# Optimization experiments

Measured on AMD Instinct MI355X. Metric: run time of the kernel, lower is better.

Reference implementation:

```python
import jax, jax.numpy as jnp
import numpy as np

N_NODES = 50000
N_EDGES = 800000
D_IN = 128
D_OUT = 128
NUM_RELS = 100


def setup_inputs() -> dict:
    key = jax.random.key(0)
    k1, k2, k3, k4, k5, k6, k7 = jax.random.split(key, 7)
    h = jax.random.normal(k1, (N_NODES, D_IN), dtype=jnp.float32)
    W = jax.random.normal(k2, (D_IN, D_OUT), dtype=jnp.float32) * 0.05
    attn = jax.random.normal(k3, (2 * D_OUT,), dtype=jnp.float32) * 0.05
    rel_emb = jax.random.normal(k4, (NUM_RELS, 1), dtype=jnp.float32)
    src = jax.random.randint(k5, (N_EDGES,), 0, N_NODES, dtype=jnp.int32)
    dst = jax.random.randint(k6, (N_EDGES,), 0, N_NODES, dtype=jnp.int32)
    etype = jax.random.randint(k7, (N_EDGES,), 0, NUM_RELS, dtype=jnp.int32)
    return {"h": h, "W": W, "attn": attn, "rel_emb": rel_emb,
            "src": src, "dst": dst, "etype": etype}


def reference(h, W, attn, rel_emb, src, dst, etype):
    # h: [N, d_in], W: [d_in, d_out], attn: [2*d_out], rel_emb: [R, 1]
    # src/dst/etype: [E]
    N = h.shape[0]
    d = W.shape[1]
    # padding_idx=0 in nn.Embedding -> row 0 is zero
    rel_table = rel_emb.at[0].set(0.0)
    z = h @ W  # [N, d_out]
    # attn_fc([z_src, z_dst]) = z_src @ a_l + z_dst @ a_r (split the concat-linear)
    s_src = z @ attn[:d]  # [N]
    s_dst = z @ attn[d:]  # [N]
    e = jax.nn.leaky_relu(s_src[src] + s_dst[dst])  # [E], slope 0.01 as in torch
    # segment softmax over incoming edges of each dst node
    m = jax.ops.segment_max(e, dst, num_segments=N)  # [N]
    ex = jnp.exp(e - m[dst])  # [E]
    denom = jax.ops.segment_sum(ex, dst, num_segments=N)  # [N]
    alpha = ex / denom[dst]  # [E]
    coef = rel_table[etype, 0] * alpha  # [E]  (rel_alpha * alpha)
    # weighted sum of source messages per destination node
    out = jax.ops.segment_sum(coef[:, None] * z[src], dst, num_segments=N)  # [N, d_out]
    return out
```

## Files before the change

kernel.cpp:

```cpp
#include <hip/hip_runtime.h>

#define D 128
#define GROWS 64
#define SPLIT 16
#define NPP (256 / SPLIT)
#define MAXPART 512

typedef __attribute__((ext_vector_type(8))) short short8;
typedef __attribute__((ext_vector_type(4))) float float4v;

__device__ __forceinline__ ushort f2bf(float x) {
    uint u = __float_as_uint(x);
    return (ushort)((u + 0x7FFFu + ((u >> 16) & 1u)) >> 16);
}
__device__ __forceinline__ float bf_lo(uint u) { return __uint_as_float(u << 16); }
__device__ __forceinline__ float bf_hi(uint u) { return __uint_as_float(u & 0xFFFF0000u); }

__global__ __launch_bounds__(256) void convW_kernel(
    const float* __restrict__ W, ushort* __restrict__ Wtg)
{
    int idx = blockIdx.x * 256 + threadIdx.x;
    int k = idx >> 7, n = idx & 127;
    Wtg[n * 128 + k] = f2bf(W[idx]);
}

__global__ __launch_bounds__(512) void gemm_mfma_kernel(
    const float* __restrict__ h, const ushort* __restrict__ Wtg,
    const float* __restrict__ attn, const int* __restrict__ dst,
    ushort* __restrict__ zb, float* __restrict__ s_src, float* __restrict__ s_dst,
    int* __restrict__ histm, int nhi, int N, int E, int nblocks)
{
    __shared__ ushort ht[GROWS * 136];
    __shared__ float psum_s[GROWS][2];
    __shared__ float psum_d[GROWS][2];
    __shared__ int histA[256];
    const int tid = threadIdx.x;
    const int base = blockIdx.x * GROWS;

#pragma unroll
    for (int it = 0; it < 4; ++it) {
        int idx = it * 512 + tid;
        int r = idx >> 5, c4 = (idx & 31) * 4;
        float4 v = make_float4(0.f, 0.f, 0.f, 0.f);
        if (base + r < N) v = *(const float4*)&h[(size_t)(base + r) * D + c4];
        ushort4 u = make_ushort4(f2bf(v.x), f2bf(v.y), f2bf(v.z), f2bf(v.w));
        *(ushort4*)&ht[r * 136 + c4] = u;
    }
    if (tid < 256) histA[tid] = 0;
    __syncthreads();

    const int lane = tid & 63;
    const int wave = tid >> 6;
    const int wr = wave >> 1;
    const int wc = wave & 1;
    const int col = lane & 15;
    const int quad = lane >> 4;
    const int wm = wr * 16;

    float4v acc[4];
#pragma unroll
    for (int nt = 0; nt < 4; ++nt) acc[nt] = (float4v)(0.f);

#pragma unroll
    for (int kc = 0; kc < 128; kc += 32) {
        short8 a = *(const short8*)&ht[(wm + col) * 136 + kc + quad * 8];
#pragma unroll
        for (int nt = 0; nt < 4; ++nt) {
            short8 b = *(const short8*)&Wtg[(wc * 64 + nt * 16 + col) * 128 + kc + quad * 8];
            acc[nt] = __builtin_amdgcn_mfma_f32_16x16x32_bf16(a, b, acc[nt], 0, 0, 0);
        }
    }
    __syncthreads();

    float ps[4] = {0.f, 0.f, 0.f, 0.f}, pd[4] = {0.f, 0.f, 0.f, 0.f};
#pragma unroll
    for (int nt = 0; nt < 4; ++nt) {
        float aL = attn[wc * 64 + nt * 16 + col];
        float aR = attn[D + wc * 64 + nt * 16 + col];
#pragma unroll
        for (int reg = 0; reg < 4; ++reg) {
            float v = acc[nt][reg];
            ps[reg] = fmaf(v, aL, ps[reg]);
            pd[reg] = fmaf(v, aR, pd[reg]);
            ht[(wm + quad * 4 + reg) * 136 + wc * 64 + nt * 16 + col] = f2bf(v);
        }
    }
#pragma unroll
    for (int reg = 0; reg < 4; ++reg) {
#pragma unroll
        for (int off = 1; off < 16; off <<= 1) {
            ps[reg] += __shfl_xor(ps[reg], off);
            pd[reg] += __shfl_xor(pd[reg], off);
        }
        if (col == 0) {
            int rl = wm + quad * 4 + reg;
            psum_s[rl][wc] = ps[reg];
            psum_d[rl][wc] = pd[reg];
        }
    }
    __syncthreads();

    if (tid < GROWS && base + tid < N) {
        s_src[base + tid] = psum_s[tid][0] + psum_s[tid][1];
        s_dst[base + tid] = psum_d[tid][0] + psum_d[tid][1];
    }

#pragma unroll
    for (int it = 0; it < 2; ++it) {
        int idx = it * 512 + tid;
        int r = idx >> 4, c8 = idx & 15;
        if (base + r < N)
            *(uint4*)&zb[(size_t)(base + r) * D + c8 * 8] = *(uint4*)&ht[r * 136 + c8 * 8];
    }

    const int cpb = (E + nblocks - 1) / nblocks;
    const int cs = blockIdx.x * cpb;
    const int ce = min(cs + cpb, E);
    for (int i = cs + tid; i < ce; i += 512)
        atomicAdd(&histA[dst[i] >> 8], 1);
    __syncthreads();
    if (tid < nhi) histm[blockIdx.x * nhi + tid] = histA[tid];
}

__global__ __launch_bounds__(64) void binB1_kernel(
    int* __restrict__ histm, int* __restrict__ colsum, int nhi, int nchunk)
{
    const int b = blockIdx.x;
    const int t = threadIdx.x;
    const int K = (nchunk + 63) / 64;
    int v[16];
    int s = 0;
#pragma unroll
    for (int j = 0; j < 16; ++j) {
        int c = t * K + j;
        v[j] = (j < K && c < nchunk) ? histm[c * nhi + b] : 0;
        s += v[j];
    }
    int incl = s;
#pragma unroll
    for (int off = 1; off < 64; off <<= 1) {
        int u = __shfl_up(incl, off);
        if (t >= off) incl += u;
    }
    int run = incl - s;
#pragma unroll
    for (int j = 0; j < 16; ++j) {
        int c = t * K + j;
        if (j < K && c < nchunk) { histm[c * nhi + b] = run; run += v[j]; }
    }
    if (t == 63) colsum[b] = incl;
}

__device__ __forceinline__ void scan_colsum_wave0(
    const int* __restrict__ colsum, int* sbase, int nhi, int lane)
{
    int v[4];
    int s = 0;
#pragma unroll
    for (int j = 0; j < 4; ++j) {
        int c = lane * 4 + j;
        v[j] = (c < nhi) ? colsum[c] : 0;
        s += v[j];
    }
    int incl = s;
#pragma unroll
    for (int off = 1; off < 64; off <<= 1) {
        int u = __shfl_up(incl, off);
        if (lane >= off) incl += u;
    }
    int run = incl - s;
#pragma unroll
    for (int j = 0; j < 4; ++j) {
        run += v[j];
        sbase[lane * 4 + j] = run;
    }
}

__global__ __launch_bounds__(256) void binC_kernel(
    const int* __restrict__ src, const int* __restrict__ dst,
    const int* __restrict__ etype, const int* __restrict__ histm,
    const int* __restrict__ colsum, uint* __restrict__ binned,
    int nhi, int E, int nchunk)
{
    __shared__ int sbase[256];
    __shared__ int cur[256];
    const int tid = threadIdx.x;
    if (tid < 64) scan_colsum_wave0(colsum, sbase, nhi, tid);
    __syncthreads();
    if (tid < nhi)
        cur[tid] = ((tid == 0) ? 0 : sbase[tid - 1]) + histm[blockIdx.x * nhi + tid];
    __syncthreads();
    const int cpb = (E + nchunk - 1) / nchunk;
    const int cs = blockIdx.x * cpb;
    const int ce = min(cs + cpb, E);
    for (int i = cs + tid; i < ce; i += 256) {
        int d = dst[i];
        int pos = atomicAdd(&cur[d >> 8], 1);
        binned[pos] = (uint)src[i] | ((uint)etype[i] << 16) | ((uint)(d & 255) << 23);
    }
}

__global__ __launch_bounds__(256) void aggD_kernel(
    const uint* __restrict__ zb32, const float* __restrict__ s_src,
    const float* __restrict__ s_dst, const int* __restrict__ colsum,
    const uint* __restrict__ binned, const float* __restrict__ rel_emb,
    float* __restrict__ out, int nhi, int N, int R)
{
    __shared__ float rel_l[128];
    __shared__ int sbase[256];
    __shared__ int hist[NPP];
    __shared__ int loff[NPP + 1];
    __shared__ int cur[NPP];
    __shared__ uint sE[MAXPART];
    __shared__ float sW[MAXPART];
    __shared__ float sDst[NPP];
    __shared__ float sDen[NPP];
    const int tid = threadIdx.x;
    const int lane = tid & 63;
    const int wave = tid >> 6;

    if (tid < R) rel_l[tid] = (tid == 0) ? 0.f : rel_emb[tid];
    if (wave == 0) scan_colsum_wave0(colsum, sbase, nhi, lane);
    if (tid < NPP) { hist[tid] = 0; sDen[tid] = 0.f; }
    __syncthreads();

    const int hi = blockIdx.x / SPLIT;
    const int part = blockIdx.x % SPLIT;
    const int bb = (hi == 0) ? 0 : sbase[hi - 1];
    const int be = sbase[hi];
    const int lobase = part * NPP;
    const int dbase = hi * 256 + lobase;

    if (tid < NPP) {
        int dd = dbase + tid;
        sDst[tid] = (dd < N) ? s_dst[dd] : 0.f;
    }

    for (int i = bb + tid; i < be; i += 256) {
        int li = (int)((binned[i] >> 23) & 0xFF) - lobase;
        if ((unsigned)li < NPP) atomicAdd(&hist[li], 1);
    }
    __syncthreads();
    if (wave == 0 && lane < NPP) {
        int hc = hist[lane];
        int incl = hc;
#pragma unroll
        for (int off = 1; off < NPP; off <<= 1) {
            int u = __shfl_up(incl, off);
            if (lane >= off) incl += u;
        }
        loff[lane + 1] = incl;
        if (lane == 0) loff[0] = 0;
        cur[lane] = incl - hc;
    }
    __syncthreads();
    for (int i = bb + tid; i < be; i += 256) {
        uint pk = binned[i];
        int li = (int)((pk >> 23) & 0xFF) - lobase;
        if ((unsigned)li < NPP) {
            int pos = atomicAdd(&cur[li], 1);
            if (pos < MAXPART) sE[pos] = pk;
        }
    }
    __syncthreads();

    const int ne = min(loff[NPP], MAXPART);
    for (int i = tid; i < ne; i += 256) {
        uint pk = sE[i];
        int srcv = (int)(pk & 0xFFFF);
        int et = (int)((pk >> 16) & 0x7F);
        int li = (int)((pk >> 23) & 0xFF) - lobase;
        float x = s_src[srcv] + sDst[li];
        float e = (x > 0.f) ? x : 0.01f * x;
        float p = __expf(e);
        sW[i] = p * rel_l[et];
        atomicAdd(&sDen[li], p);
    }
    __syncthreads();

    const int q = lane >> 4;
    const int ql = lane & 15;
    const int nIdx = wave * 4 + q;
    const int d = dbase + nIdx;
    if (d >= N) return;

    const int st = min(loff[nIdx], MAXPART);
    const int en = min(loff[nIdx + 1], MAXPART);
    const float den = sDen[nIdx];
    const float inv = (den > 0.f) ? 1.0f / den : 0.f;

    float4 acc0 = make_float4(0.f, 0.f, 0.f, 0.f);
    float4 acc1 = make_float4(0.f, 0.f, 0.f, 0.f);

    for (int b2 = st; b2 < en; b2 += 8) {
        float w[8];
        int sv[8];
#pragma unroll
        for (int j = 0; j < 8; ++j) {
            int idx = b2 + j;
            bool valid = idx < en;
            w[j] = valid ? sW[idx] : 0.f;
            sv[j] = valid ? (int)(sE[idx] & 0xFFFF) : 0;
        }
        uint4 u[8];
#pragma unroll
        for (int j = 0; j < 8; ++j)
            u[j] = *(const uint4*)(zb32 + (size_t)sv[j] * 64 + ql * 4);
#pragma unroll
        for (int j = 0; j < 8; ++j) {
            const float wj = w[j];
            acc0.x = fmaf(wj, bf_lo(u[j].x), acc0.x);
            acc0.y = fmaf(wj, bf_hi(u[j].x), acc0.y);
            acc0.z = fmaf(wj, bf_lo(u[j].y), acc0.z);
            acc0.w = fmaf(wj, bf_hi(u[j].y), acc0.w);
            acc1.x = fmaf(wj, bf_lo(u[j].z), acc1.x);
            acc1.y = fmaf(wj, bf_hi(u[j].z), acc1.y);
            acc1.z = fmaf(wj, bf_lo(u[j].w), acc1.z);
            acc1.w = fmaf(wj, bf_hi(u[j].w), acc1.w);
        }
    }

    float* orow = out + (size_t)d * D + ql * 8;
    *(float4*)orow       = make_float4(acc0.x * inv, acc0.y * inv, acc0.z * inv, acc0.w * inv);
    *(float4*)(orow + 4) = make_float4(acc1.x * inv, acc1.y * inv, acc1.z * inv, acc1.w * inv);
}

extern "C" void kernel_launch(void* const* d_in, const int* in_sizes, int n_in,
                              void* d_out, int out_size, void* d_ws, size_t ws_size,
                              hipStream_t stream)
{
    const float* h    = (const float*)d_in[0];
    const float* W    = (const float*)d_in[1];
    const float* attn = (const float*)d_in[2];
    const float* rel  = (const float*)d_in[3];
    const int*   src  = (const int*)d_in[4];
    const int*   dst  = (const int*)d_in[5];
    const int*   et   = (const int*)d_in[6];
    float* out = (float*)d_out;

    const int N = in_sizes[0] / D;
    const int E = in_sizes[4];
    const int R = in_sizes[3];

    char* p = (char*)d_ws;
    auto alloc = [&](size_t bytes) {
        char* q = p;
        p += (bytes + 255) & ~(size_t)255;
        return q;
    };
    const int nhi     = (N + 255) / 256;
    const int gblocks = (N + GROWS - 1) / GROWS;

    ushort* zb     = (ushort*)alloc((size_t)N * D * sizeof(ushort));
    ushort* Wtg    = (ushort*)alloc((size_t)D * D * sizeof(ushort));
    float* ssrc    = (float*)alloc((size_t)N * sizeof(float));
    float* sdst    = (float*)alloc((size_t)N * sizeof(float));
    uint*  binned  = (uint*)alloc((size_t)E * sizeof(uint));
    int*   histm   = (int*)alloc((size_t)gblocks * nhi * sizeof(int));
    int*   colsum  = (int*)alloc((size_t)nhi * sizeof(int));

    convW_kernel<<<64, 256, 0, stream>>>(W, Wtg);
    gemm_mfma_kernel<<<gblocks, 512, 0, stream>>>(h, Wtg, attn, dst, zb, ssrc, sdst,
                                                  histm, nhi, N, E, gblocks);
    binB1_kernel<<<nhi, 64, 0, stream>>>(histm, colsum, nhi, gblocks);
    binC_kernel<<<gblocks, 256, 0, stream>>>(src, dst, et, histm, colsum, binned,
                                             nhi, E, gblocks);
    aggD_kernel<<<nhi * SPLIT, 256, 0, stream>>>((const uint*)zb, ssrc, sdst,
                                                 colsum, binned, rel, out, nhi, N, R);
}
```

Measured before the change: 182.7 us.

## Split aggregation into a per-bin sort kernel and a per-node gather kernel

The old aggregation kernel launched 16 blocks per 256-node destination bin. Each block rescanned the whole bin twice and kept its slice in shared memory, capped at 512 edges. The new binD kernel processes each bin once: it counts edges per node, computes global per-node offsets, writes edges sorted by node as (src, weight) pairs, and stores each node's inverse softmax denominator. A separate aggE kernel then gathers z rows per destination node straight from that global sorted array. This removes the 16x redundant bin scans and the 512-edge truncation, at the cost of an extra launch, an 8-byte-per-edge global write and read, and a sort stage that runs on only one block per bin.

```diff
diff --git a/kernel.cpp b/kernel.cpp
--- a/kernel.cpp
+++ b/kernel.cpp
@@ -2,9 +2,6 @@
 
 #define D 128
 #define GROWS 64
-#define SPLIT 16
-#define NPP (256 / SPLIT)
-#define MAXPART 512
 
 typedef __attribute__((ext_vector_type(8))) short short8;
 typedef __attribute__((ext_vector_type(4))) float float4v;
@@ -200,115 +197,121 @@
     }
 }
 
-__global__ __launch_bounds__(256) void aggD_kernel(
-    const uint* __restrict__ zb32, const float* __restrict__ s_src,
+__global__ __launch_bounds__(256) void binD_kernel(
+    const uint* __restrict__ binned, const float* __restrict__ s_src,
     const float* __restrict__ s_dst, const int* __restrict__ colsum,
-    const uint* __restrict__ binned, const float* __restrict__ rel_emb,
-    float* __restrict__ out, int nhi, int N, int R)
+    const float* __restrict__ rel_emb, uint2* __restrict__ sorted,
+    int* __restrict__ nodeoff, float* __restrict__ nodeInv,
+    int nhi, int N, int R)
 {
     __shared__ float rel_l[128];
     __shared__ int sbase[256];
-    __shared__ int hist[NPP];
-    __shared__ int loff[NPP + 1];
-    __shared__ int cur[NPP];
-    __shared__ uint sE[MAXPART];
-    __shared__ float sW[MAXPART];
-    __shared__ float sDst[NPP];
-    __shared__ float sDen[NPP];
+    __shared__ int hist[256];
+    __shared__ int loff[257];
+    __shared__ int cur[256];
+    __shared__ float sDst[256];
+    __shared__ float sDen[256];
+    __shared__ int wsum[4];
     const int tid = threadIdx.x;
     const int lane = tid & 63;
     const int wave = tid >> 6;
 
     if (tid < R) rel_l[tid] = (tid == 0) ? 0.f : rel_emb[tid];
     if (wave == 0) scan_colsum_wave0(colsum, sbase, nhi, lane);
-    if (tid < NPP) { hist[tid] = 0; sDen[tid] = 0.f; }
-    __syncthreads();
-
-    const int hi = blockIdx.x / SPLIT;
-    const int part = blockIdx.x % SPLIT;
+    hist[tid] = 0;
+    sDen[tid] = 0.f;
+    const int hi = blockIdx.x;
+    const int dbase = hi * 256;
+    {
+        int dd = dbase + tid;
+        sDst[tid] = (dd < N) ? s_dst[dd] : 0.f;
+    }
+    __syncthreads();
+
     const int bb = (hi == 0) ? 0 : sbase[hi - 1];
     const int be = sbase[hi];
-    const int lobase = part * NPP;
-    const int dbase = hi * 256 + lobase;
-
-    if (tid < NPP) {
-        int dd = dbase + tid;
-        sDst[tid] = (dd < N) ? s_dst[dd] : 0.f;
-    }
-
-    for (int i = bb + tid; i < be; i += 256) {
-        int li = (int)((binned[i] >> 23) & 0xFF) - lobase;
-        if ((unsigned)li < NPP) atomicAdd(&hist[li], 1);
-    }
-    __syncthreads();
-    if (wave == 0 && lane < NPP) {
-        int hc = hist[lane];
-        int incl = hc;
-#pragma unroll
-        for (int off = 1; off < NPP; off <<= 1) {
+
+    for (int i = bb + tid; i < be; i += 256)
+        atomicAdd(&hist[(binned[i] >> 23) & 0xFF], 1);
+    __syncthreads();
+
+    {
+        int v = hist[tid];
+        int incl = v;
+#pragma unroll
+        for (int off = 1; off < 64; off <<= 1) {
             int u = __shfl_up(incl, off);
             if (lane >= off) incl += u;
         }
-        loff[lane + 1] = incl;
-        if (lane == 0) loff[0] = 0;
-        cur[lane] = incl - hc;
-    }
-    __syncthreads();
+        if (lane == 63) wsum[wave] = incl;
+        __syncthreads();
+        int woff = 0;
+#pragma unroll
+        for (int w = 0; w < 4; ++w)
+            if (w < wave) woff += wsum[w];
+        incl += woff;
+        loff[tid + 1] = incl;
+        if (tid == 0) loff[0] = 0;
+        int excl = incl - v;
+        cur[tid] = excl;
+        nodeoff[dbase + tid] = bb + excl;
+    }
+    __syncthreads();
+
     for (int i = bb + tid; i < be; i += 256) {
         uint pk = binned[i];
-        int li = (int)((pk >> 23) & 0xFF) - lobase;
-        if ((unsigned)li < NPP) {
-            int pos = atomicAdd(&cur[li], 1);
-            if (pos < MAXPART) sE[pos] = pk;
-        }
-    }
-    __syncthreads();
-
-    const int ne = min(loff[NPP], MAXPART);
-    for (int i = tid; i < ne; i += 256) {
-        uint pk = sE[i];
         int srcv = (int)(pk & 0xFFFF);
         int et = (int)((pk >> 16) & 0x7F);
-        int li = (int)((pk >> 23) & 0xFF) - lobase;
+        int li = (int)((pk >> 23) & 0xFF);
         float x = s_src[srcv] + sDst[li];
         float e = (x > 0.f) ? x : 0.01f * x;
         float p = __expf(e);
-        sW[i] = p * rel_l[et];
+        int pos = bb + atomicAdd(&cur[li], 1);
+        sorted[pos] = make_uint2((uint)srcv, __float_as_uint(p * rel_l[et]));
         atomicAdd(&sDen[li], p);
     }
     __syncthreads();
 
+    {
+        float den = sDen[tid];
+        nodeInv[dbase + tid] = (den > 0.f) ? 1.0f / den : 0.f;
+    }
+}
+
+__global__ __launch_bounds__(256) void aggE_kernel(
+    const uint* __restrict__ zb32, const uint2* __restrict__ sorted,
+    const int* __restrict__ nodeoff, const float* __restrict__ nodeInv,
+    float* __restrict__ out, int N)
+{
+    const int tid = threadIdx.x;
+    const int lane = tid & 63;
+    const int wave = tid >> 6;
     const int q = lane >> 4;
     const int ql = lane & 15;
-    const int nIdx = wave * 4 + q;
-    const int d = dbase + nIdx;
+    const int d = blockIdx.x * 16 + wave * 4 + q;
     if (d >= N) return;
 
-    const int st = min(loff[nIdx], MAXPART);
-    const int en = min(loff[nIdx + 1], MAXPART);
-    const float den = sDen[nIdx];
-    const float inv = (den > 0.f) ? 1.0f / den : 0.f;
+    const int st = nodeoff[d];
+    const int en = nodeoff[d + 1];
+    const float inv = nodeInv[d];
 
     float4 acc0 = make_float4(0.f, 0.f, 0.f, 0.f);
     float4 acc1 = make_float4(0.f, 0.f, 0.f, 0.f);
 
     for (int b2 = st; b2 < en; b2 += 8) {
-        float w[8];
-        int sv[8];
+        uint2 hdr[8];
 #pragma unroll
         for (int j = 0; j < 8; ++j) {
             int idx = b2 + j;
-            bool valid = idx < en;
-            w[j] = valid ? sW[idx] : 0.f;
-            sv[j] = valid ? (int)(sE[idx] & 0xFFFF) : 0;
+            hdr[j] = (idx < en) ? sorted[idx] : make_uint2(0u, 0u);
         }
         uint4 u[8];
 #pragma unroll
         for (int j = 0; j < 8; ++j)
-            u[j] = *(const uint4*)(zb32 + (size_t)sv[j] * 64 + ql * 4);
+            u[j] = *(const uint4*)(zb32 + (size_t)hdr[j].x * 64 + ql * 4);
 #pragma unroll
         for (int j = 0; j < 8; ++j) {
-            const float wj = w[j];
+            const float wj = __uint_as_float(hdr[j].y);
             acc0.x = fmaf(wj, bf_lo(u[j].x), acc0.x);
             acc0.y = fmaf(wj, bf_hi(u[j].x), acc0.y);
             acc0.z = fmaf(wj, bf_lo(u[j].y), acc0.z);
@@ -351,13 +354,16 @@
     const int nhi     = (N + 255) / 256;
     const int gblocks = (N + GROWS - 1) / GROWS;
 
-    ushort* zb     = (ushort*)alloc((size_t)N * D * sizeof(ushort));
-    ushort* Wtg    = (ushort*)alloc((size_t)D * D * sizeof(ushort));
-    float* ssrc    = (float*)alloc((size_t)N * sizeof(float));
-    float* sdst    = (float*)alloc((size_t)N * sizeof(float));
-    uint*  binned  = (uint*)alloc((size_t)E * sizeof(uint));
-    int*   histm   = (int*)alloc((size_t)gblocks * nhi * sizeof(int));
-    int*   colsum  = (int*)alloc((size_t)nhi * sizeof(int));
+    ushort* zb      = (ushort*)alloc((size_t)N * D * sizeof(ushort));
+    ushort* Wtg     = (ushort*)alloc((size_t)D * D * sizeof(ushort));
+    float* ssrc     = (float*)alloc((size_t)N * sizeof(float));
+    float* sdst     = (float*)alloc((size_t)N * sizeof(float));
+    uint*  binned   = (uint*)alloc((size_t)E * sizeof(uint));
+    int*   histm    = (int*)alloc((size_t)gblocks * nhi * sizeof(int));
+    int*   colsum   = (int*)alloc((size_t)nhi * sizeof(int));
+    uint2* sorted   = (uint2*)alloc((size_t)E * sizeof(uint2));
+    int*   nodeoff  = (int*)alloc(((size_t)nhi * 256 + 1) * sizeof(int));
+    float* nodeInv  = (float*)alloc((size_t)nhi * 256 * sizeof(float));
 
     convW_kernel<<<64, 256, 0, stream>>>(W, Wtg);
     gemm_mfma_kernel<<<gblocks, 512, 0, stream>>>(h, Wtg, attn, dst, zb, ssrc, sdst,
@@ -365,6 +371,8 @@
     binB1_kernel<<<nhi, 64, 0, stream>>>(histm, colsum, nhi, gblocks);
     binC_kernel<<<gblocks, 256, 0, stream>>>(src, dst, et, histm, colsum, binned,
                                              nhi, E, gblocks);
-    aggD_kernel<<<nhi * SPLIT, 256, 0, stream>>>((const uint*)zb, ssrc, sdst,
-                                                 colsum, binned, rel, out, nhi, N, R);
-}
+    binD_kernel<<<nhi, 256, 0, stream>>>(binned, ssrc, sdst, colsum, rel,
+                                         sorted, nodeoff, nodeInv, nhi, N, R);
+    aggE_kernel<<<(N + 15) / 16, 256, 0, stream>>>((const uint*)zb, sorted,
+                                                   nodeoff, nodeInv, out, N);
+}
```

Result: faster. 171.0 us (-6.4%).
